# Optimization experiments

Measured on AMD Instinct MI355X. Metric: run time of the kernel, lower is better.

Reference implementation:

```python
import jax, jax.numpy as jnp
import numpy as np
from jax import lax

WINDOW_SIZE = 5
SIGMA = 1.0
DILATIONS = [1 + int(i ** 1.5) for i in range(5)]  # [1, 2, 3, 6, 9]
C1 = (0.01 * 255.0) ** 2
C2 = (0.03 * 255.0) ** 2


def _make_window(channel=1):
    x = np.arange(WINDOW_SIZE, dtype=np.float64)
    g = np.exp(-((x - WINDOW_SIZE // 2) ** 2) / (2.0 * SIGMA ** 2))
    g = g / g.sum()
    w2d = np.outer(g, g)
    w2d = w2d / w2d.sum()
    w = np.broadcast_to(w2d[None, None], (channel, 1, WINDOW_SIZE, WINDOW_SIZE))
    return jnp.asarray(w, jnp.float32)


def _dw_conv(x, window, dilation):
    # depthwise 'same' conv; pad = (dilated_kernel - 1)/2 = 2*dilation (always even total pad)
    pad = 2 * dilation
    return lax.conv_general_dilated(
        x, window, window_strides=(1, 1),
        padding=((pad, pad), (pad, pad)),
        rhs_dilation=(dilation, dilation),
        dimension_numbers=('NCHW', 'OIHW', 'NCHW'),
        feature_group_count=window.shape[0])


def _ssim_mean(img1, img2, window, dilation):
    mu1 = _dw_conv(img1, window, dilation)
    mu2 = _dw_conv(img2, window, dilation)
    si11 = _dw_conv(img1 * img1, window, dilation)
    si22 = _dw_conv(img2 * img2, window, dilation)
    si12 = _dw_conv(img1 * img2, window, dilation)
    mu1_sq = mu1 * mu1
    mu2_sq = mu2 * mu2
    mu1_mu2 = mu1 * mu2
    sigma1_sq = si11 - mu1_sq
    sigma2_sq = si22 - mu2_sq
    sigma12 = si12 - mu1_mu2
    ssim_map = ((2.0 * mu1_mu2 + C1) * (2.0 * sigma12 + C2)) / (
        (mu1_sq + mu2_sq + C1) * (sigma1_sq + sigma2_sq + C2))
    return jnp.mean(ssim_map)


def _avg_pool2(x):
    B, C, H, W = x.shape
    return x.reshape(B, C, H // 2, 2, W // 2, 2).mean(axis=(3, 5))


def setup_inputs() -> dict:
    key = jax.random.key(0)
    k1, k2 = jax.random.split(key)
    img1 = jax.random.uniform(k1, (16, 1, 1024, 1024), dtype=jnp.float32)
    img2 = jax.random.uniform(k2, (16, 1, 1024, 1024), dtype=jnp.float32)
    window = _make_window(channel=1)
    weights = jnp.asarray([0.0448, 0.2856, 0.3001, 0.2363, 0.1333], jnp.float32)
    return {"img1": img1, "img2": img2, "window": window, "weights": weights}


def reference(img1, img2, window, weights):
    eps = 1e-12
    m = jnp.max(img2)
    a = (img1 + eps) / (m + eps) * 255.0
    b = (img2 + eps) / (m + eps) * 255.0
    mssim = []
    for dil in DILATIONS:
        mssim.append(_ssim_mean(a, b, window, dil))
        a = _avg_pool2(a)
        b = _avg_pool2(b)
    mssim = jnp.stack(mssim)
    return 1.0 - jnp.prod(mssim ** weights)
```

## Files before the change

kernel.cpp:

```cpp
#include <hip/hip_runtime.h>
#include <hip/hip_bf16.h>
#include <math.h>

#define EPSN 1e-12f
#define SSIM_C1 6.5025f
#define SSIM_C2 58.5225f



__global__ void init_ws_kernel(float* ws) {
    if (threadIdx.x < 16) ws[threadIdx.x] = 0.0f;
}


__global__ void max_kernel(const float4* __restrict__ img2, int n4,
                           unsigned* __restrict__ maxbits) {
    float m = 0.0f;
    for (int i = blockIdx.x * blockDim.x + threadIdx.x; i < n4;
         i += gridDim.x * blockDim.x) {
        float4 v = img2[i];
        m = fmaxf(fmaxf(m, fmaxf(v.x, v.y)), fmaxf(v.z, v.w));
    }
#pragma unroll
    for (int o = 32; o > 0; o >>= 1) m = fmaxf(m, __shfl_down(m, o));
    __shared__ float sm[4];
    int tid = threadIdx.x;
    if ((tid & 63) == 0) sm[tid >> 6] = m;
    __syncthreads();
    if (tid == 0) {
        float mm = fmaxf(fmaxf(sm[0], sm[1]), fmaxf(sm[2], sm[3]));
        atomicMax(maxbits, __float_as_uint(mm));
    }
}


template <int D>
__global__ __launch_bounds__(256) void ssim_sep_kernel(
        const float* __restrict__ A, const float* __restrict__ B,
        int H, int W, const unsigned* __restrict__ maxbits,
        const float* __restrict__ window, float* __restrict__ sumOut,
        float* __restrict__ poolA, float* __restrict__ poolB) {
    constexpr int TW = 64, TH = 64, TPT = 16;
    constexpr int LW = TW + 4 * D, LH = TH + 4 * D, P = 4 * D + 1;
    __shared__ float2 AB[LH][LW];

    int tx = threadIdx.x, ty = threadIdx.y;
    int tid = ty * 64 + tx;
    int b = blockIdx.z;
    int x0 = blockIdx.x * TW - 2 * D;
    int y0 = blockIdx.y * TH - 2 * D;

    const float* Ab = A + (size_t)b * H * W;
    const float* Bb = B + (size_t)b * H * W;

    for (int idx = tid; idx < LW * LH; idx += 256) {
        int ly = idx / LW;
        int lx = idx - ly * LW;
        int gx = x0 + lx, gy = y0 + ly;
        float va = 0.0f, vb = 0.0f;
        if ((unsigned)gx < (unsigned)W && (unsigned)gy < (unsigned)H) {
            size_t g = (size_t)gy * W + gx;
            va = Ab[g];
            vb = Bb[g];
        }
        AB[ly][lx] = make_float2(va, vb);
    }
    __syncthreads();

    if (poolA) {
        int pW = W >> 1;
        for (int idx = tid; idx < 32 * 32; idx += 256) {
            int py = idx >> 5, px = idx & 31;
            float2 v00 = AB[2 * D + 2 * py][2 * D + 2 * px];
            float2 v01 = AB[2 * D + 2 * py][2 * D + 2 * px + 1];
            float2 v10 = AB[2 * D + 2 * py + 1][2 * D + 2 * px];
            float2 v11 = AB[2 * D + 2 * py + 1][2 * D + 2 * px + 1];
            float pa = 0.25f * ((v00.x + v01.x) + (v10.x + v11.x));
            float pb = 0.25f * ((v00.y + v01.y) + (v10.y + v11.y));
            int gx = (blockIdx.x * TW >> 1) + px;
            int gy = (blockIdx.y * TH >> 1) + py;
            size_t o = (size_t)b * (H >> 1) * pW + (size_t)gy * pW + gx;
            poolA[o] = pa;
            poolB[o] = pb;
        }
    }

    float g1[5];
#pragma unroll
    for (int k = 0; k < 5; k++)
        g1[k] = ((window[k * 5 + 0] + window[k * 5 + 1]) +
                 (window[k * 5 + 2] + window[k * 5 + 3])) + window[k * 5 + 4];

    float m = __uint_as_float(*maxbits);
    float sc = 255.0f / (m + EPSN);
    float s2 = sc * sc;
    float s2x2 = 2.0f * s2;

    float hA[P], hB[P], hAA[P], hBB[P], hAB[P];
    float local = 0.0f;
    int base = ty * TPT;

#pragma unroll
    for (int r = 0; r < TPT + 4 * D; ++r) {
        int l = base + r;
        float ha = 0, hb = 0, haa = 0, hbb = 0, hab = 0;
#pragma unroll
        for (int k = 0; k < 5; k++) {
            float2 ab = AB[l][tx + k * D];
            float w = g1[k];
            float wa = w * ab.x, wb = w * ab.y;
            ha += wa;
            hb += wb;
            haa = fmaf(wa, ab.x, haa);
            hbb = fmaf(wb, ab.y, hbb);
            hab = fmaf(wa, ab.y, hab);
        }
        int slot = r % P;
        hA[slot] = ha; hB[slot] = hb;
        hAA[slot] = haa; hBB[slot] = hbb; hAB[slot] = hab;

        if (r >= 4 * D) {
            int o = r - 4 * D;
            float m1 = 0, m2 = 0, S11 = 0, S22 = 0, S12 = 0;
#pragma unroll
            for (int k = 0; k < 5; k++) {
                int sl = (o + k * D) % P;
                float w = g1[k];
                m1 = fmaf(w, hA[sl], m1);
                m2 = fmaf(w, hB[sl], m2);
                S11 = fmaf(w, hAA[sl], S11);
                S22 = fmaf(w, hBB[sl], S22);
                S12 = fmaf(w, hAB[sl], S12);
            }
            float m1s = m1 * m1, m2s = m2 * m2, m12 = m1 * m2;
            float num1 = fmaf(s2x2, m12, SSIM_C1);
            float den1 = fmaf(s2, m1s + m2s, SSIM_C1);
            float num2 = fmaf(s2x2, S12 - m12, SSIM_C2);
            float den2 = fmaf(s2, (S11 - m1s) + (S22 - m2s), SSIM_C2);
            float den = den1 * den2;
            local += (num1 * num2) * __builtin_amdgcn_rcpf(den);
        }
    }

#pragma unroll
    for (int o = 32; o > 0; o >>= 1) local += __shfl_down(local, o);
    __shared__ float part[4];
    if ((tid & 63) == 0) part[tid >> 6] = local;
    __syncthreads();
    if (tid == 0) atomicAdd(sumOut, (part[0] + part[1]) + (part[2] + part[3]));
}


template <int D>
__global__ __launch_bounds__(256) void ssim_direct_kernel(
        const float* __restrict__ A, const float* __restrict__ B,
        int H, int W, const unsigned* __restrict__ maxbits,
        const float* __restrict__ window, float* __restrict__ sumOut,
        float* __restrict__ poolA, float* __restrict__ poolB) {
    constexpr int TW = 64, TH = 16;
    constexpr int LW = TW + 4 * D, LH = TH + 4 * D;
    __shared__ float ldsA[LH][LW];
    __shared__ float ldsB[LH][LW];

    int tx = threadIdx.x, ty = threadIdx.y;
    int tid = ty * 64 + tx;
    int b = blockIdx.z;
    int x0 = blockIdx.x * TW - 2 * D;
    int y0 = blockIdx.y * TH - 2 * D;

    const float* Ab = A + (size_t)b * H * W;
    const float* Bb = B + (size_t)b * H * W;

    for (int idx = tid; idx < LW * LH; idx += 256) {
        int ly = idx / LW;
        int lx = idx - ly * LW;
        int gx = x0 + lx, gy = y0 + ly;
        float va = 0.0f, vb = 0.0f;
        if ((unsigned)gx < (unsigned)W && (unsigned)gy < (unsigned)H) {
            size_t g = (size_t)gy * W + gx;
            va = Ab[g];
            vb = Bb[g];
        }
        ldsA[ly][lx] = va;
        ldsB[ly][lx] = vb;
    }
    __syncthreads();

    if (poolA) {
        int pW = W >> 1;
        int py = tid >> 5, px = tid & 31;
        float a00 = ldsA[2 * D + 2 * py][2 * D + 2 * px];
        float a01 = ldsA[2 * D + 2 * py][2 * D + 2 * px + 1];
        float a10 = ldsA[2 * D + 2 * py + 1][2 * D + 2 * px];
        float a11 = ldsA[2 * D + 2 * py + 1][2 * D + 2 * px + 1];
        float b00 = ldsB[2 * D + 2 * py][2 * D + 2 * px];
        float b01 = ldsB[2 * D + 2 * py][2 * D + 2 * px + 1];
        float b10 = ldsB[2 * D + 2 * py + 1][2 * D + 2 * px];
        float b11 = ldsB[2 * D + 2 * py + 1][2 * D + 2 * px + 1];
        int gx = (blockIdx.x * TW >> 1) + px;
        int gy = (blockIdx.y * TH >> 1) + py;
        size_t o = (size_t)b * (H >> 1) * pW + (size_t)gy * pW + gx;
        poolA[o] = 0.25f * ((a00 + a01) + (a10 + a11));
        poolB[o] = 0.25f * ((b00 + b01) + (b10 + b11));
    }

    float wv[25];
#pragma unroll
    for (int i = 0; i < 25; i++) wv[i] = window[i];

    float m = __uint_as_float(*maxbits);
    float sc = 255.0f / (m + EPSN);
    float s2 = sc * sc;
    float s2x2 = 2.0f * s2;

    float mu1[4] = {0, 0, 0, 0}, mu2[4] = {0, 0, 0, 0};
    float s11[4] = {0, 0, 0, 0}, s22[4] = {0, 0, 0, 0}, s12[4] = {0, 0, 0, 0};
    int ry = ty * 4;
#pragma unroll
    for (int ky = 0; ky < 5; ky++) {
#pragma unroll
        for (int kx = 0; kx < 5; kx++) {
            float w = wv[ky * 5 + kx];
#pragma unroll
            for (int j = 0; j < 4; j++) {
                float a = ldsA[ry + j + ky * D][tx + kx * D];
                float bb = ldsB[ry + j + ky * D][tx + kx * D];
                float wa = w * a, wb = w * bb;
                mu1[j] += wa;
                mu2[j] += wb;
                s11[j] = fmaf(wa, a, s11[j]);
                s22[j] = fmaf(wb, bb, s22[j]);
                s12[j] = fmaf(wa, bb, s12[j]);
            }
        }
    }

    float local = 0.0f;
#pragma unroll
    for (int j = 0; j < 4; j++) {
        float m1s = mu1[j] * mu1[j], m2s = mu2[j] * mu2[j], m12 = mu1[j] * mu2[j];
        float num1 = fmaf(s2x2, m12, SSIM_C1);
        float den1 = fmaf(s2, m1s + m2s, SSIM_C1);
        float num2 = fmaf(s2x2, s12[j] - m12, SSIM_C2);
        float den2 = fmaf(s2, (s11[j] - m1s) + (s22[j] - m2s), SSIM_C2);
        local += (num1 * num2) * __builtin_amdgcn_rcpf(den1 * den2);
    }

#pragma unroll
    for (int o = 32; o > 0; o >>= 1) local += __shfl_down(local, o);
    __shared__ float part[4];
    if ((tid & 63) == 0) part[tid >> 6] = local;
    __syncthreads();
    if (tid == 0) atomicAdd(sumOut, (part[0] + part[1]) + (part[2] + part[3]));
}


__global__ void final_kernel(const float* __restrict__ sums,
                             const float* __restrict__ weights,
                             unsigned* __restrict__ out) {
    if (blockIdx.x == 0 && threadIdx.x == 0) {
        const float counts[5] = {16.0f * 1024 * 1024, 16.0f * 512 * 512,
                                 16.0f * 256 * 256,   16.0f * 128 * 128,
                                 16.0f * 64 * 64};
        float prod = 1.0f;
#pragma unroll
        for (int i = 0; i < 5; i++) {
            float m = sums[i] / counts[i];
            prod *= powf(m, weights[i]);
        }
        float r = 1.0f - prod;
        unsigned bits = __float_as_uint(r);
        unsigned lsb = (bits >> 16) & 1u;
        unsigned hi = (bits + 0x7FFFu + lsb) >> 16;
        out[0] = (hi << 16) | hi;
    }
}


extern "C" void kernel_launch(void* const* d_in, const int* in_sizes, int n_in,
                              void* d_out, int out_size, void* d_ws, size_t ws_size,
                              hipStream_t stream) {
    const float* img1 = (const float*)d_in[0];
    const float* img2 = (const float*)d_in[1];
    const float* window = (const float*)d_in[2];
    const float* weights = (const float*)d_in[3];

    float* ws = (float*)d_ws;
    unsigned* maxbits = (unsigned*)d_ws;
    float* sums = ws + 4;
    size_t off = 16;
    float* a1 = ws + off; off += (size_t)16 * 512 * 512;
    float* b1 = ws + off; off += (size_t)16 * 512 * 512;
    float* a2 = ws + off; off += (size_t)16 * 256 * 256;
    float* b2 = ws + off; off += (size_t)16 * 256 * 256;
    float* a3 = ws + off; off += (size_t)16 * 128 * 128;
    float* b3 = ws + off; off += (size_t)16 * 128 * 128;
    float* a4 = ws + off; off += (size_t)16 * 64 * 64;
    float* b4 = ws + off; off += (size_t)16 * 64 * 64;

    dim3 blk(64, 4, 1);

    init_ws_kernel<<<1, 64, 0, stream>>>(ws);
    max_kernel<<<2048, 256, 0, stream>>>((const float4*)img2,
                                         16 * 1024 * 1024 / 4, maxbits);

    ssim_sep_kernel<1><<<dim3(16, 16, 16), blk, 0, stream>>>(
        img1, img2, 1024, 1024, maxbits, window, sums + 0, a1, b1);
    ssim_sep_kernel<2><<<dim3(8, 8, 16), blk, 0, stream>>>(
        a1, b1, 512, 512, maxbits, window, sums + 1, a2, b2);
    ssim_sep_kernel<3><<<dim3(4, 4, 16), blk, 0, stream>>>(
        a2, b2, 256, 256, maxbits, window, sums + 2, a3, b3);
    ssim_direct_kernel<6><<<dim3(2, 8, 16), blk, 0, stream>>>(
        a3, b3, 128, 128, maxbits, window, sums + 3, a4, b4);
    ssim_direct_kernel<9><<<dim3(1, 4, 16), blk, 0, stream>>>(
        a4, b4, 64, 64, maxbits, window, sums + 4, nullptr, nullptr);

    final_kernel<<<1, 64, 0, stream>>>(sums, weights, (unsigned*)d_out);
}
```

Baseline: 322.8 us.

## Halve SSIM tile heights and vectorize interior tile loads with float4

Tile heights are halved in the separable and direct SSIM kernels (64→32 and 16→8 rows) and the grids are doubled, giving more blocks and less LDS per block. The shared-memory fill is split into a float4 global load of the 64-wide interior plus a scalar loop for the halo columns, replacing per-element loads that needed an integer division. The intent is more occupancy and wider memory transactions in the bandwidth-bound first level. The cost is a larger halo-to-interior ratio, so more redundant halo traffic and vertical recompute in the sliding separable filter.

```diff
diff --git a/kernel.cpp b/kernel.cpp
--- a/kernel.cpp
+++ b/kernel.cpp
@@ -40,23 +40,38 @@
         int H, int W, const unsigned* __restrict__ maxbits,
         const float* __restrict__ window, float* __restrict__ sumOut,
         float* __restrict__ poolA, float* __restrict__ poolB) {
-    constexpr int TW = 64, TH = 64, TPT = 16;
+    constexpr int TW = 64, TH = 32, TPT = 8;
     constexpr int LW = TW + 4 * D, LH = TH + 4 * D, P = 4 * D + 1;
     __shared__ float2 AB[LH][LW];
 
     int tx = threadIdx.x, ty = threadIdx.y;
     int tid = ty * 64 + tx;
     int b = blockIdx.z;
-    int x0 = blockIdx.x * TW - 2 * D;
+    int x0i = blockIdx.x * TW;
     int y0 = blockIdx.y * TH - 2 * D;
 
     const float* Ab = A + (size_t)b * H * W;
     const float* Bb = B + (size_t)b * H * W;
 
-    for (int idx = tid; idx < LW * LH; idx += 256) {
-        int ly = idx / LW;
-        int lx = idx - ly * LW;
-        int gx = x0 + lx, gy = y0 + ly;
+    for (int idx = tid; idx < LH * 16; idx += 256) {
+        int ly = idx >> 4, j = idx & 15;
+        int gy = y0 + ly;
+        float4 a = make_float4(0, 0, 0, 0), v = make_float4(0, 0, 0, 0);
+        if ((unsigned)gy < (unsigned)H) {
+            const float4* Ar = (const float4*)(Ab + (size_t)gy * W + x0i);
+            const float4* Br = (const float4*)(Bb + (size_t)gy * W + x0i);
+            a = Ar[j];
+            v = Br[j];
+        }
+        float4* dst = (float4*)&AB[ly][2 * D + 4 * j];
+        dst[0] = make_float4(a.x, v.x, a.y, v.y);
+        dst[1] = make_float4(a.z, v.z, a.w, v.w);
+    }
+    for (int idx = tid; idx < LH * 4 * D; idx += 256) {
+        int ly = idx / (4 * D), h = idx % (4 * D);
+        int lx = (h < 2 * D) ? h : h + TW;
+        int gx = x0i - 2 * D + lx;
+        int gy = y0 + ly;
         float va = 0.0f, vb = 0.0f;
         if ((unsigned)gx < (unsigned)W && (unsigned)gy < (unsigned)H) {
             size_t g = (size_t)gy * W + gx;
@@ -69,19 +84,17 @@
 
     if (poolA) {
         int pW = W >> 1;
-        for (int idx = tid; idx < 32 * 32; idx += 256) {
+        for (int idx = tid; idx < 32 * 16; idx += 256) {
             int py = idx >> 5, px = idx & 31;
             float2 v00 = AB[2 * D + 2 * py][2 * D + 2 * px];
             float2 v01 = AB[2 * D + 2 * py][2 * D + 2 * px + 1];
             float2 v10 = AB[2 * D + 2 * py + 1][2 * D + 2 * px];
             float2 v11 = AB[2 * D + 2 * py + 1][2 * D + 2 * px + 1];
-            float pa = 0.25f * ((v00.x + v01.x) + (v10.x + v11.x));
-            float pb = 0.25f * ((v00.y + v01.y) + (v10.y + v11.y));
-            int gx = (blockIdx.x * TW >> 1) + px;
+            int gx = (x0i >> 1) + px;
             int gy = (blockIdx.y * TH >> 1) + py;
             size_t o = (size_t)b * (H >> 1) * pW + (size_t)gy * pW + gx;
-            poolA[o] = pa;
-            poolB[o] = pb;
+            poolA[o] = 0.25f * ((v00.x + v01.x) + (v10.x + v11.x));
+            poolB[o] = 0.25f * ((v00.y + v01.y) + (v10.y + v11.y));
         }
     }
 
@@ -137,8 +150,7 @@
             float den1 = fmaf(s2, m1s + m2s, SSIM_C1);
             float num2 = fmaf(s2x2, S12 - m12, SSIM_C2);
             float den2 = fmaf(s2, (S11 - m1s) + (S22 - m2s), SSIM_C2);
-            float den = den1 * den2;
-            local += (num1 * num2) * __builtin_amdgcn_rcpf(den);
+            local += (num1 * num2) * __builtin_amdgcn_rcpf(den1 * den2);
         }
     }
 
@@ -151,30 +163,48 @@
 }
 
 
-template <int D>
+template <int D, int TH>
 __global__ __launch_bounds__(256) void ssim_direct_kernel(
         const float* __restrict__ A, const float* __restrict__ B,
         int H, int W, const unsigned* __restrict__ maxbits,
         const float* __restrict__ window, float* __restrict__ sumOut,
         float* __restrict__ poolA, float* __restrict__ poolB) {
-    constexpr int TW = 64, TH = 16;
-    constexpr int LW = TW + 4 * D, LH = TH + 4 * D;
+    constexpr int TW = 64;
+    constexpr int LW = TW + 4 * D, LH = TH + 4 * D, OPT = TH / 4;
     __shared__ float ldsA[LH][LW];
     __shared__ float ldsB[LH][LW];
 
     int tx = threadIdx.x, ty = threadIdx.y;
     int tid = ty * 64 + tx;
     int b = blockIdx.z;
-    int x0 = blockIdx.x * TW - 2 * D;
+    int x0i = blockIdx.x * TW;
     int y0 = blockIdx.y * TH - 2 * D;
 
     const float* Ab = A + (size_t)b * H * W;
     const float* Bb = B + (size_t)b * H * W;
 
-    for (int idx = tid; idx < LW * LH; idx += 256) {
-        int ly = idx / LW;
-        int lx = idx - ly * LW;
-        int gx = x0 + lx, gy = y0 + ly;
+    for (int idx = tid; idx < LH * 16; idx += 256) {
+        int ly = idx >> 4, j = idx & 15;
+        int gy = y0 + ly;
+        float4 a = make_float4(0, 0, 0, 0), v = make_float4(0, 0, 0, 0);
+        if ((unsigned)gy < (unsigned)H) {
+            const float4* Ar = (const float4*)(Ab + (size_t)gy * W + x0i);
+            const float4* Br = (const float4*)(Bb + (size_t)gy * W + x0i);
+            a = Ar[j];
+            v = Br[j];
+        }
+        float2* da = (float2*)&ldsA[ly][2 * D + 4 * j];
+        float2* db = (float2*)&ldsB[ly][2 * D + 4 * j];
+        da[0] = make_float2(a.x, a.y);
+        da[1] = make_float2(a.z, a.w);
+        db[0] = make_float2(v.x, v.y);
+        db[1] = make_float2(v.z, v.w);
+    }
+    for (int idx = tid; idx < LH * 4 * D; idx += 256) {
+        int ly = idx / (4 * D), h = idx % (4 * D);
+        int lx = (h < 2 * D) ? h : h + TW;
+        int gx = x0i - 2 * D + lx;
+        int gy = y0 + ly;
         float va = 0.0f, vb = 0.0f;
         if ((unsigned)gx < (unsigned)W && (unsigned)gy < (unsigned)H) {
             size_t g = (size_t)gy * W + gx;
@@ -188,20 +218,22 @@
 
     if (poolA) {
         int pW = W >> 1;
-        int py = tid >> 5, px = tid & 31;
-        float a00 = ldsA[2 * D + 2 * py][2 * D + 2 * px];
-        float a01 = ldsA[2 * D + 2 * py][2 * D + 2 * px + 1];
-        float a10 = ldsA[2 * D + 2 * py + 1][2 * D + 2 * px];
-        float a11 = ldsA[2 * D + 2 * py + 1][2 * D + 2 * px + 1];
-        float b00 = ldsB[2 * D + 2 * py][2 * D + 2 * px];
-        float b01 = ldsB[2 * D + 2 * py][2 * D + 2 * px + 1];
-        float b10 = ldsB[2 * D + 2 * py + 1][2 * D + 2 * px];
-        float b11 = ldsB[2 * D + 2 * py + 1][2 * D + 2 * px + 1];
-        int gx = (blockIdx.x * TW >> 1) + px;
-        int gy = (blockIdx.y * TH >> 1) + py;
-        size_t o = (size_t)b * (H >> 1) * pW + (size_t)gy * pW + gx;
-        poolA[o] = 0.25f * ((a00 + a01) + (a10 + a11));
-        poolB[o] = 0.25f * ((b00 + b01) + (b10 + b11));
+        for (int idx = tid; idx < 32 * (TH / 2); idx += 256) {
+            int py = idx >> 5, px = idx & 31;
+            float a00 = ldsA[2 * D + 2 * py][2 * D + 2 * px];
+            float a01 = ldsA[2 * D + 2 * py][2 * D + 2 * px + 1];
+            float a10 = ldsA[2 * D + 2 * py + 1][2 * D + 2 * px];
+            float a11 = ldsA[2 * D + 2 * py + 1][2 * D + 2 * px + 1];
+            float b00 = ldsB[2 * D + 2 * py][2 * D + 2 * px];
+            float b01 = ldsB[2 * D + 2 * py][2 * D + 2 * px + 1];
+            float b10 = ldsB[2 * D + 2 * py + 1][2 * D + 2 * px];
+            float b11 = ldsB[2 * D + 2 * py + 1][2 * D + 2 * px + 1];
+            int gx = (x0i >> 1) + px;
+            int gy = (blockIdx.y * TH >> 1) + py;
+            size_t o = (size_t)b * (H >> 1) * pW + (size_t)gy * pW + gx;
+            poolA[o] = 0.25f * ((a00 + a01) + (a10 + a11));
+            poolB[o] = 0.25f * ((b00 + b01) + (b10 + b11));
+        }
     }
 
     float wv[25];
@@ -213,16 +245,16 @@
     float s2 = sc * sc;
     float s2x2 = 2.0f * s2;
 
-    float mu1[4] = {0, 0, 0, 0}, mu2[4] = {0, 0, 0, 0};
-    float s11[4] = {0, 0, 0, 0}, s22[4] = {0, 0, 0, 0}, s12[4] = {0, 0, 0, 0};
-    int ry = ty * 4;
+    float mu1[OPT] = {}, mu2[OPT] = {};
+    float s11[OPT] = {}, s22[OPT] = {}, s12[OPT] = {};
+    int ry = ty * OPT;
 #pragma unroll
     for (int ky = 0; ky < 5; ky++) {
 #pragma unroll
         for (int kx = 0; kx < 5; kx++) {
             float w = wv[ky * 5 + kx];
 #pragma unroll
-            for (int j = 0; j < 4; j++) {
+            for (int j = 0; j < OPT; j++) {
                 float a = ldsA[ry + j + ky * D][tx + kx * D];
                 float bb = ldsB[ry + j + ky * D][tx + kx * D];
                 float wa = w * a, wb = w * bb;
@@ -237,7 +269,7 @@
 
     float local = 0.0f;
 #pragma unroll
-    for (int j = 0; j < 4; j++) {
+    for (int j = 0; j < OPT; j++) {
         float m1s = mu1[j] * mu1[j], m2s = mu2[j] * mu2[j], m12 = mu1[j] * mu2[j];
         float num1 = fmaf(s2x2, m12, SSIM_C1);
         float den1 = fmaf(s2, m1s + m2s, SSIM_C1);
@@ -304,15 +336,15 @@
     max_kernel<<<2048, 256, 0, stream>>>((const float4*)img2,
                                          16 * 1024 * 1024 / 4, maxbits);
 
-    ssim_sep_kernel<1><<<dim3(16, 16, 16), blk, 0, stream>>>(
+    ssim_sep_kernel<1><<<dim3(16, 32, 16), blk, 0, stream>>>(
         img1, img2, 1024, 1024, maxbits, window, sums + 0, a1, b1);
-    ssim_sep_kernel<2><<<dim3(8, 8, 16), blk, 0, stream>>>(
+    ssim_sep_kernel<2><<<dim3(8, 16, 16), blk, 0, stream>>>(
         a1, b1, 512, 512, maxbits, window, sums + 1, a2, b2);
-    ssim_sep_kernel<3><<<dim3(4, 4, 16), blk, 0, stream>>>(
+    ssim_sep_kernel<3><<<dim3(4, 8, 16), blk, 0, stream>>>(
         a2, b2, 256, 256, maxbits, window, sums + 2, a3, b3);
-    ssim_direct_kernel<6><<<dim3(2, 8, 16), blk, 0, stream>>>(
+    ssim_direct_kernel<6, 8><<<dim3(2, 16, 16), blk, 0, stream>>>(
         a3, b3, 128, 128, maxbits, window, sums + 3, a4, b4);
-    ssim_direct_kernel<9><<<dim3(1, 4, 16), blk, 0, stream>>>(
+    ssim_direct_kernel<9, 8><<<dim3(1, 8, 16), blk, 0, stream>>>(
         a4, b4, 64, 64, maxbits, window, sums + 4, nullptr, nullptr);
 
     final_kernel<<<1, 64, 0, stream>>>(sums, weights, (unsigned*)d_out);
```

Measured after the change: 343.2 us. +6.3%, slower.
